# Performance work log

Hardware: AMD Instinct MI355X
Metric: run time of the kernel (lower is better)

The kernel has to match this reference:

```python
import jax, jax.numpy as jnp
import numpy as np

# Modulated deformable conv2d (torchvision semantics): per kernel tap, sample the
# input at a runtime-offset location via bilinear interpolation (zero padding
# outside the image), modulate with mask, then do the weighted accumulation.

STRIDE = (1, 1)
PADDING = (1, 1)
DILATION = (1, 1)


def deform_conv2d(x, offset, mask, weight, bias):
    B, C, H, W = x.shape
    O, Cg, kh, kw = weight.shape
    K = kh * kw
    og = offset.shape[1] // (2 * K)          # offset groups
    Ho, Wo = offset.shape[2], offset.shape[3]
    sh, sw = STRIDE
    ph, pw = PADDING
    dh, dw = DILATION

    off = offset.reshape(B, og, K, 2, Ho, Wo)
    ki = jnp.arange(K)
    base_ky = ((ki // kw) * dh).astype(x.dtype)            # [K]
    base_kx = ((ki % kw) * dw).astype(x.dtype)
    base_h = (jnp.arange(Ho) * sh - ph).astype(x.dtype)    # [Ho]
    base_w = (jnp.arange(Wo) * sw - pw).astype(x.dtype)    # [Wo]
    # sampling positions, [B, og, K, Ho, Wo]
    p_y = off[:, :, :, 0] + base_ky[None, None, :, None, None] + base_h[None, None, None, :, None]
    p_x = off[:, :, :, 1] + base_kx[None, None, :, None, None] + base_w[None, None, None, None, :]

    y0 = jnp.floor(p_y)
    x0 = jnp.floor(p_x)
    ly = p_y - y0
    lx = p_x - x0
    y0i = y0.astype(jnp.int32)
    x0i = x0.astype(jnp.int32)

    Cog = C // og
    x_flat = x.reshape(B, og, Cog, H * W)

    def gather(yi, xi):
        valid = ((yi >= 0) & (yi < H) & (xi >= 0) & (xi < W))
        idx = jnp.clip(yi, 0, H - 1) * W + jnp.clip(xi, 0, W - 1)
        idx_flat = idx.reshape(B, og, 1, K * Ho * Wo)
        v = jnp.take_along_axis(x_flat, idx_flat, axis=3).reshape(B, og, Cog, K, Ho, Wo)
        return v * valid[:, :, None].astype(x.dtype)

    w00 = ((1 - ly) * (1 - lx))[:, :, None]
    w01 = ((1 - ly) * lx)[:, :, None]
    w10 = (ly * (1 - lx))[:, :, None]
    w11 = (ly * lx)[:, :, None]
    val = (w00 * gather(y0i, x0i) + w01 * gather(y0i, x0i + 1)
           + w10 * gather(y0i + 1, x0i) + w11 * gather(y0i + 1, x0i + 1))

    if mask is not None:
        val = val * mask.reshape(B, og, K, Ho, Wo)[:, :, None]

    # grouped conv accumulation over sampled taps
    G = C // Cg                               # conv groups (=1 here)
    val = val.reshape(B, G, C // G, K, Ho, Wo)
    w = weight.reshape(G, O // G, Cg, K)
    out = jnp.einsum('bgckhw,gock->bgohw', val, w).reshape(B, O, Ho, Wo)
    if bias is not None:
        out = out + bias[None, :, None, None]
    return out


def setup_inputs() -> dict:
    key = jax.random.key(0)
    k1, k2, k3, k4, k5 = jax.random.split(key, 5)
    B, C, H, W = 4, 64, 128, 128
    O, kh, kw = 64, 3, 3
    return {
        'input': jax.random.normal(k1, (B, C, H, W), dtype=jnp.float32),
        'offset': jax.random.normal(k2, (B, 2 * kh * kw, H, W), dtype=jnp.float32),
        'mask': jax.random.uniform(k3, (B, kh * kw, H, W), dtype=jnp.float32),
        'weight': jax.random.normal(k4, (O, C, kh, kw), dtype=jnp.float32) * (1.0 / np.sqrt(C * kh * kw)),
        'bias': jax.random.normal(k5, (O,), dtype=jnp.float32) * 0.01,
    }


def reference(input, offset, mask, weight, bias):
    return deform_conv2d(input, offset, mask, weight, bias)
```

## Files before the change

### kernel.cpp

```cpp
#include <hip/hip_runtime.h>


#define BB 4
#define CC 64
#define HH 128
#define WW 128
#define OO 64
#define KHW 3
#define KK 9
#define HW (HH * WW)

typedef __bf16 bf16_t;
typedef bf16_t bf16x8 __attribute__((ext_vector_type(8)));
typedef float f32x4 __attribute__((ext_vector_type(4)));

__global__ __launch_bounds__(256) void nhwc_kernel(const float* __restrict__ x,
                                                   bf16_t* __restrict__ xt) {
    __shared__ float tile[64 * 65];
    const int t  = threadIdx.x;
    const int b  = blockIdx.x >> 8;
    const int p0 = (blockIdx.x & 255) << 6;
#pragma unroll
    for (int i = 0; i < 16; ++i) {
        int c = i * 4 + (t >> 6);
        int p = t & 63;
        tile[c * 65 + p] = x[(b * CC + c) * HW + p0 + p];
    }
    __syncthreads();
#pragma unroll
    for (int i = 0; i < 16; ++i) {
        int p = i * 4 + (t >> 6);
        int c = t & 63;
        xt[(size_t)((b * HW) + p0 + p) * CC + c] = (bf16_t)tile[c * 65 + p];
    }
}

__global__ void wfrag_kernel(const float* __restrict__ w,
                             bf16_t* __restrict__ wf) {
    int i = blockIdx.x * blockDim.x + threadIdx.x;
    if (i >= OO * CC * KK) return;
    int j    = i & 7;
    int lane = (i >> 3) & 63;
    int nt   = (i >> 9) & 3;
    int q    = (i >> 11) & 1;
    int k    = i >> 12;
    int o = nt * 16 + (lane & 15);
    int c = q * 32 + ((lane >> 4) << 3) + j;
    wf[i] = (bf16_t)w[(o * CC + c) * KK + k];
}

__global__ __launch_bounds__(256) void deform_conv_mfma(
    const bf16_t* __restrict__ xt, const float* __restrict__ offset,
    const float* __restrict__ mask, const bf16x8* __restrict__ wf,
    const float* __restrict__ bias, float* __restrict__ out) {
    const int t    = threadIdx.x;
    const int b    = blockIdx.x >> 8;
    const int p0   = (blockIdx.x & 255) << 6;
    const int lane = t & 63;
    const int wv   = t >> 6;
    const int m0   = wv << 4;
    const int col  = lane & 15;
    const int quad = lane >> 4;
    const int rem  = p0 + m0 + col;
    const int ho   = rem >> 7;
    const int wo   = rem & (WW - 1);
    const int cb   = quad << 3;

    const bf16_t* xb  = xt + (size_t)b * HW * CC;
    const float* offp = offset + (size_t)b * (2 * KK) * HW + rem;
    const float* mp   = mask + (size_t)b * KK * HW + rem;

    f32x4 acc[4];
#pragma unroll
    for (int nt = 0; nt < 4; ++nt) acc[nt] = (f32x4){0.f, 0.f, 0.f, 0.f};

    float offy = offp[0];
    float offx = offp[HW];
    float mm   = mp[0];

    for (int k = 0; k < KK; ++k) {
        float n_offy = 0.f, n_offx = 0.f, n_mm = 0.f;
        if (k < KK - 1) {
            n_offy = offp[(2 * k + 2) * HW];
            n_offx = offp[(2 * k + 3) * HW];
            n_mm   = mp[(k + 1) * HW];
        }

        float py = offy + (float)(k / KHW) + (float)(ho - 1);
        float px = offx + (float)(k % KHW) + (float)(wo - 1);
        float fy0 = floorf(py), fx0 = floorf(px);
        float ly = py - fy0, lx = px - fx0;
        int y0 = (int)fy0, x0 = (int)fx0;
        int y1 = y0 + 1, x1 = x0 + 1;
        bool vy0 = (y0 >= 0) && (y0 < HH);
        bool vy1 = (y1 >= 0) && (y1 < HH);
        bool vx0 = (x0 >= 0) && (x0 < WW);
        bool vx1 = (x1 >= 0) && (x1 < WW);
        int cy0 = min(max(y0, 0), HH - 1), cy1 = min(max(y1, 0), HH - 1);
        int cx0 = min(max(x0, 0), WW - 1), cx1 = min(max(x1, 0), WW - 1);
        float w0 = (vy0 && vx0) ? mm * (1.0f - ly) * (1.0f - lx) : 0.0f;
        float w1 = (vy0 && vx1) ? mm * (1.0f - ly) * lx : 0.0f;
        float w2 = (vy1 && vx0) ? mm * ly * (1.0f - lx) : 0.0f;
        float w3 = (vy1 && vx1) ? mm * ly * lx : 0.0f;

        const bf16_t* b00 = xb + (size_t)(cy0 * WW + cx0) * CC + cb;
        const bf16_t* b01 = xb + (size_t)(cy0 * WW + cx1) * CC + cb;
        const bf16_t* b10 = xb + (size_t)(cy1 * WW + cx0) * CC + cb;
        const bf16_t* b11 = xb + (size_t)(cy1 * WW + cx1) * CC + cb;
        bf16x8 a00 = *(const bf16x8*)b00, c00 = *(const bf16x8*)(b00 + 32);
        bf16x8 a01 = *(const bf16x8*)b01, c01 = *(const bf16x8*)(b01 + 32);
        bf16x8 a10 = *(const bf16x8*)b10, c10 = *(const bf16x8*)(b10 + 32);
        bf16x8 a11 = *(const bf16x8*)b11, c11 = *(const bf16x8*)(b11 + 32);

        bf16x8 af0, af1;
#pragma unroll
        for (int i = 0; i < 8; ++i) {
            float v = w0 * (float)a00[i] + w1 * (float)a01[i] +
                      w2 * (float)a10[i] + w3 * (float)a11[i];
            af0[i] = (bf16_t)v;
        }
#pragma unroll
        for (int i = 0; i < 8; ++i) {
            float v = w0 * (float)c00[i] + w1 * (float)c01[i] +
                      w2 * (float)c10[i] + w3 * (float)c11[i];
            af1[i] = (bf16_t)v;
        }

#pragma unroll
        for (int nt = 0; nt < 4; ++nt) {
            bf16x8 bfg = wf[(k * 8 + nt) * 64 + lane];
            acc[nt] = __builtin_amdgcn_mfma_f32_16x16x32_bf16(
                af0, bfg, acc[nt], 0, 0, 0);
        }
#pragma unroll
        for (int nt = 0; nt < 4; ++nt) {
            bf16x8 bfg = wf[(k * 8 + 4 + nt) * 64 + lane];
            acc[nt] = __builtin_amdgcn_mfma_f32_16x16x32_bf16(
                af1, bfg, acc[nt], 0, 0, 0);
        }

        offy = n_offy;
        offx = n_offx;
        mm   = n_mm;
    }

#pragma unroll
    for (int nt = 0; nt < 4; ++nt) {
        int o = nt * 16 + col;
        float bv = bias[o];
        f32x4 r = acc[nt];
        r.x += bv; r.y += bv; r.z += bv; r.w += bv;
        float* dst = out + (size_t)(b * OO + o) * HW + p0 + m0 + quad * 4;
        *(f32x4*)dst = r;
    }
}

extern "C" void kernel_launch(void* const* d_in, const int* in_sizes, int n_in,
                              void* d_out, int out_size, void* d_ws,
                              size_t ws_size, hipStream_t stream) {
    const float* x      = (const float*)d_in[0];
    const float* offset = (const float*)d_in[1];
    const float* mask   = (const float*)d_in[2];
    const float* weight = (const float*)d_in[3];
    const float* bias   = (const float*)d_in[4];
    float* out = (float*)d_out;

    bf16_t* xt  = (bf16_t*)d_ws;
    bf16_t* wfr = (bf16_t*)((char*)d_ws + (size_t)BB * HW * CC * 2);

    nhwc_kernel<<<BB * (HW / 64), 256, 0, stream>>>(x, xt);

    int nw = OO * CC * KK;
    wfrag_kernel<<<(nw + 255) / 256, 256, 0, stream>>>(weight, wfr);

    deform_conv_mfma<<<BB * (HW / 64), 256, 0, stream>>>(
        xt, offset, mask, (const bf16x8*)wfr, bias, out);
}
```

Measured before the change: 122.6 us.

## Split channel halves across wave pairs with LDS reduction; merge prep kernels

The main kernel now runs 512 threads per block, and each pair of waves splits the 64 input channels into two halves. Each wave gathers and interpolates only 32 channels and issues half the MFMAs, so more waves are available to hide gather latency. Partial accumulators are summed through shared memory before the bias add and store. The NHWC transpose and the weight-fragment kernels are also fused into one launch to save launch overhead. The cost is duplicated offset and mask loads and bilinear weight math per wave pair, plus a block-wide sync and LDS traffic.

Measured after the change: 126.4 us. 3.0% more time.

```diff
diff --git a/kernel.cpp b/kernel.cpp
--- a/kernel.cpp
+++ b/kernel.cpp
@@ -14,57 +14,60 @@
 typedef bf16_t bf16x8 __attribute__((ext_vector_type(8)));
 typedef float f32x4 __attribute__((ext_vector_type(4)));
 
-__global__ __launch_bounds__(256) void nhwc_kernel(const float* __restrict__ x,
-                                                   bf16_t* __restrict__ xt) {
+__global__ __launch_bounds__(256) void prep_kernel(const float* __restrict__ x,
+                                                   bf16_t* __restrict__ xt,
+                                                   const float* __restrict__ w,
+                                                   bf16_t* __restrict__ wf) {
     __shared__ float tile[64 * 65];
-    const int t  = threadIdx.x;
-    const int b  = blockIdx.x >> 8;
-    const int p0 = (blockIdx.x & 255) << 6;
+    const int t = threadIdx.x;
+    if (blockIdx.x < BB * 256) {
+        const int b  = blockIdx.x >> 8;
+        const int p0 = (blockIdx.x & 255) << 6;
 #pragma unroll
-    for (int i = 0; i < 16; ++i) {
-        int c = i * 4 + (t >> 6);
-        int p = t & 63;
-        tile[c * 65 + p] = x[(b * CC + c) * HW + p0 + p];
-    }
-    __syncthreads();
+        for (int i = 0; i < 16; ++i) {
+            int c = i * 4 + (t >> 6);
+            int p = t & 63;
+            tile[c * 65 + p] = x[(b * CC + c) * HW + p0 + p];
+        }
+        __syncthreads();
 #pragma unroll
-    for (int i = 0; i < 16; ++i) {
-        int p = i * 4 + (t >> 6);
-        int c = t & 63;
-        xt[(size_t)((b * HW) + p0 + p) * CC + c] = (bf16_t)tile[c * 65 + p];
+        for (int i = 0; i < 16; ++i) {
+            int p = i * 4 + (t >> 6);
+            int c = t & 63;
+            xt[(size_t)((b * HW) + p0 + p) * CC + c] = (bf16_t)tile[c * 65 + p];
+        }
+    } else {
+        int i = (blockIdx.x - BB * 256) * 256 + t;
+        if (i >= OO * CC * KK) return;
+        int j    = i & 7;
+        int lane = (i >> 3) & 63;
+        int nt   = (i >> 9) & 3;
+        int q    = (i >> 11) & 1;
+        int k    = i >> 12;
+        int o = nt * 16 + (lane & 15);
+        int c = q * 32 + ((lane >> 4) << 3) + j;
+        wf[i] = (bf16_t)w[(o * CC + c) * KK + k];
     }
 }
 
-__global__ void wfrag_kernel(const float* __restrict__ w,
-                             bf16_t* __restrict__ wf) {
-    int i = blockIdx.x * blockDim.x + threadIdx.x;
-    if (i >= OO * CC * KK) return;
-    int j    = i & 7;
-    int lane = (i >> 3) & 63;
-    int nt   = (i >> 9) & 3;
-    int q    = (i >> 11) & 1;
-    int k    = i >> 12;
-    int o = nt * 16 + (lane & 15);
-    int c = q * 32 + ((lane >> 4) << 3) + j;
-    wf[i] = (bf16_t)w[(o * CC + c) * KK + k];
-}
-
-__global__ __launch_bounds__(256) void deform_conv_mfma(
+__global__ __launch_bounds__(512, 8) void deform_conv_mfma(
     const bf16_t* __restrict__ xt, const float* __restrict__ offset,
     const float* __restrict__ mask, const bf16x8* __restrict__ wf,
     const float* __restrict__ bias, float* __restrict__ out) {
-    const int t    = threadIdx.x;
-    const int b    = blockIdx.x >> 8;
-    const int p0   = (blockIdx.x & 255) << 6;
-    const int lane = t & 63;
-    const int wv   = t >> 6;
-    const int m0   = wv << 4;
-    const int col  = lane & 15;
-    const int quad = lane >> 4;
-    const int rem  = p0 + m0 + col;
-    const int ho   = rem >> 7;
-    const int wo   = rem & (WW - 1);
-    const int cb   = quad << 3;
+    const int t     = threadIdx.x;
+    const int b     = blockIdx.x >> 8;
+    const int p0    = (blockIdx.x & 255) << 6;
+    const int lane  = t & 63;
+    const int wv    = t >> 6;
+    const int strip = wv >> 1;
+    const int q     = wv & 1;
+    const int m0    = strip << 4;
+    const int col   = lane & 15;
+    const int quad  = lane >> 4;
+    const int rem   = p0 + m0 + col;
+    const int ho    = rem >> 7;
+    const int wo    = rem & (WW - 1);
+    const int cb    = q * 32 + (quad << 3);
 
     const bf16_t* xb  = xt + (size_t)b * HW * CC;
     const float* offp = offset + (size_t)b * (2 * KK) * HW + rem;
@@ -103,40 +106,24 @@
         float w2 = (vy1 && vx0) ? mm * ly * (1.0f - lx) : 0.0f;
         float w3 = (vy1 && vx1) ? mm * ly * lx : 0.0f;
 
-        const bf16_t* b00 = xb + (size_t)(cy0 * WW + cx0) * CC + cb;
-        const bf16_t* b01 = xb + (size_t)(cy0 * WW + cx1) * CC + cb;
-        const bf16_t* b10 = xb + (size_t)(cy1 * WW + cx0) * CC + cb;
-        const bf16_t* b11 = xb + (size_t)(cy1 * WW + cx1) * CC + cb;
-        bf16x8 a00 = *(const bf16x8*)b00, c00 = *(const bf16x8*)(b00 + 32);
-        bf16x8 a01 = *(const bf16x8*)b01, c01 = *(const bf16x8*)(b01 + 32);
-        bf16x8 a10 = *(const bf16x8*)b10, c10 = *(const bf16x8*)(b10 + 32);
-        bf16x8 a11 = *(const bf16x8*)b11, c11 = *(const bf16x8*)(b11 + 32);
+        bf16x8 a00 = *(const bf16x8*)(xb + (size_t)(cy0 * WW + cx0) * CC + cb);
+        bf16x8 a01 = *(const bf16x8*)(xb + (size_t)(cy0 * WW + cx1) * CC + cb);
+        bf16x8 a10 = *(const bf16x8*)(xb + (size_t)(cy1 * WW + cx0) * CC + cb);
+        bf16x8 a11 = *(const bf16x8*)(xb + (size_t)(cy1 * WW + cx1) * CC + cb);
 
-        bf16x8 af0, af1;
+        bf16x8 af;
 #pragma unroll
         for (int i = 0; i < 8; ++i) {
             float v = w0 * (float)a00[i] + w1 * (float)a01[i] +
                       w2 * (float)a10[i] + w3 * (float)a11[i];
-            af0[i] = (bf16_t)v;
-        }
-#pragma unroll
-        for (int i = 0; i < 8; ++i) {
-            float v = w0 * (float)c00[i] + w1 * (float)c01[i] +
-                      w2 * (float)c10[i] + w3 * (float)c11[i];
-            af1[i] = (bf16_t)v;
+            af[i] = (bf16_t)v;
         }
 
 #pragma unroll
         for (int nt = 0; nt < 4; ++nt) {
-            bf16x8 bfg = wf[(k * 8 + nt) * 64 + lane];
+            bf16x8 bfg = wf[((k * 2 + q) * 4 + nt) * 64 + lane];
             acc[nt] = __builtin_amdgcn_mfma_f32_16x16x32_bf16(
-                af0, bfg, acc[nt], 0, 0, 0);
-        }
-#pragma unroll
-        for (int nt = 0; nt < 4; ++nt) {
-            bf16x8 bfg = wf[(k * 8 + 4 + nt) * 64 + lane];
-            acc[nt] = __builtin_amdgcn_mfma_f32_16x16x32_bf16(
-                af1, bfg, acc[nt], 0, 0, 0);
+                af, bfg, acc[nt], 0, 0, 0);
         }
 
         offy = n_offy;
@@ -144,14 +131,22 @@
         mm   = n_mm;
     }
 
+    __shared__ f32x4 red[4][64][4];
+    if (q) {
 #pragma unroll
-    for (int nt = 0; nt < 4; ++nt) {
-        int o = nt * 16 + col;
-        float bv = bias[o];
-        f32x4 r = acc[nt];
-        r.x += bv; r.y += bv; r.z += bv; r.w += bv;
-        float* dst = out + (size_t)(b * OO + o) * HW + p0 + m0 + quad * 4;
-        *(f32x4*)dst = r;
+        for (int nt = 0; nt < 4; ++nt) red[strip][lane][nt] = acc[nt];
+    }
+    __syncthreads();
+    if (!q) {
+#pragma unroll
+        for (int nt = 0; nt < 4; ++nt) {
+            int o = nt * 16 + col;
+            float bv = bias[o];
+            f32x4 r = acc[nt] + red[strip][lane][nt];
+            r.x += bv; r.y += bv; r.z += bv; r.w += bv;
+            float* dst = out + (size_t)(b * OO + o) * HW + p0 + m0 + quad * 4;
+            *(f32x4*)dst = r;
+        }
     }
 }
 
@@ -168,11 +163,9 @@
     bf16_t* xt  = (bf16_t*)d_ws;
     bf16_t* wfr = (bf16_t*)((char*)d_ws + (size_t)BB * HW * CC * 2);
 
-    nhwc_kernel<<<BB * (HW / 64), 256, 0, stream>>>(x, xt);
+    int nwf_blocks = (OO * CC * KK + 255) / 256;
+    prep_kernel<<<BB * 256 + nwf_blocks, 256, 0, stream>>>(x, xt, weight, wfr);
 
-    int nw = OO * CC * KK;
-    wfrag_kernel<<<(nw + 255) / 256, 256, 0, stream>>>(weight, wfr);
-
-    deform_conv_mfma<<<BB * (HW / 64), 256, 0, stream>>>(
+    deform_conv_mfma<<<BB * (HW / 64), 512, 0, stream>>>(
         xt, offset, mask, (const bf16x8*)wfr, bias, out);
 }
```

## Software-pipeline gathers across taps, merge prep kernels, swizzle block order

Applied to the files above, without the earlier changes.

Restructures the tap loop into a fully unrolled two-stage software pipeline: the bilinear gather loads for tap k+1 and the offset/mask loads for tap k+2 are issued before tap k is blended and fed to the MFMAs, so gather latency overlaps compute. It also merges the NHWC transpose and weight-fragment kernels into a single launch, adds a min-blocks-per-CU hint to launch_bounds, and reorders block indices with a stride-8 interleave. The double-buffered registers raise register pressure, which the occupancy hint may force into spills.

Result: no change. 121.5 us (-0.9%).

```diff
diff --git a/kernel.cpp b/kernel.cpp
--- a/kernel.cpp
+++ b/kernel.cpp
@@ -14,48 +14,50 @@
 typedef bf16_t bf16x8 __attribute__((ext_vector_type(8)));
 typedef float f32x4 __attribute__((ext_vector_type(4)));
 
-__global__ __launch_bounds__(256) void nhwc_kernel(const float* __restrict__ x,
-                                                   bf16_t* __restrict__ xt) {
+__global__ __launch_bounds__(256) void prep_kernel(const float* __restrict__ x,
+                                                   bf16_t* __restrict__ xt,
+                                                   const float* __restrict__ w,
+                                                   bf16_t* __restrict__ wf) {
     __shared__ float tile[64 * 65];
-    const int t  = threadIdx.x;
-    const int b  = blockIdx.x >> 8;
-    const int p0 = (blockIdx.x & 255) << 6;
-#pragma unroll
-    for (int i = 0; i < 16; ++i) {
-        int c = i * 4 + (t >> 6);
-        int p = t & 63;
-        tile[c * 65 + p] = x[(b * CC + c) * HW + p0 + p];
-    }
-    __syncthreads();
-#pragma unroll
-    for (int i = 0; i < 16; ++i) {
-        int p = i * 4 + (t >> 6);
-        int c = t & 63;
-        xt[(size_t)((b * HW) + p0 + p) * CC + c] = (bf16_t)tile[c * 65 + p];
+    const int t = threadIdx.x;
+    if (blockIdx.x < BB * 256) {
+        const int b  = blockIdx.x >> 8;
+        const int p0 = (blockIdx.x & 255) << 6;
+#pragma unroll
+        for (int i = 0; i < 16; ++i) {
+            int c = i * 4 + (t >> 6);
+            int p = t & 63;
+            tile[c * 65 + p] = x[(b * CC + c) * HW + p0 + p];
+        }
+        __syncthreads();
+#pragma unroll
+        for (int i = 0; i < 16; ++i) {
+            int p = i * 4 + (t >> 6);
+            int c = t & 63;
+            xt[(size_t)((b * HW) + p0 + p) * CC + c] = (bf16_t)tile[c * 65 + p];
+        }
+    } else {
+        int i = (blockIdx.x - BB * 256) * 256 + t;
+        if (i >= OO * CC * KK) return;
+        int j    = i & 7;
+        int lane = (i >> 3) & 63;
+        int nt   = (i >> 9) & 3;
+        int q    = (i >> 11) & 1;
+        int k    = i >> 12;
+        int o = nt * 16 + (lane & 15);
+        int c = q * 32 + ((lane >> 4) << 3) + j;
+        wf[i] = (bf16_t)w[(o * CC + c) * KK + k];
     }
 }
 
-__global__ void wfrag_kernel(const float* __restrict__ w,
-                             bf16_t* __restrict__ wf) {
-    int i = blockIdx.x * blockDim.x + threadIdx.x;
-    if (i >= OO * CC * KK) return;
-    int j    = i & 7;
-    int lane = (i >> 3) & 63;
-    int nt   = (i >> 9) & 3;
-    int q    = (i >> 11) & 1;
-    int k    = i >> 12;
-    int o = nt * 16 + (lane & 15);
-    int c = q * 32 + ((lane >> 4) << 3) + j;
-    wf[i] = (bf16_t)w[(o * CC + c) * KK + k];
-}
-
-__global__ __launch_bounds__(256) void deform_conv_mfma(
+__global__ __launch_bounds__(256, 4) void deform_conv_mfma(
     const bf16_t* __restrict__ xt, const float* __restrict__ offset,
     const float* __restrict__ mask, const bf16x8* __restrict__ wf,
     const float* __restrict__ bias, float* __restrict__ out) {
     const int t    = threadIdx.x;
-    const int b    = blockIdx.x >> 8;
-    const int p0   = (blockIdx.x & 255) << 6;
+    const int wg   = (blockIdx.x & 7) * ((BB * 256) >> 3) + (blockIdx.x >> 3);
+    const int b    = wg >> 8;
+    const int p0   = (wg & 255) << 6;
     const int lane = t & 63;
     const int wv   = t >> 6;
     const int m0   = wv << 4;
@@ -65,6 +67,8 @@
     const int ho   = rem >> 7;
     const int wo   = rem & (WW - 1);
     const int cb   = quad << 3;
+    const float fho = (float)(ho - 1);
+    const float fwo = (float)(wo - 1);
 
     const bf16_t* xb  = xt + (size_t)b * HW * CC;
     const float* offp = offset + (size_t)b * (2 * KK) * HW + rem;
@@ -74,75 +78,105 @@
 #pragma unroll
     for (int nt = 0; nt < 4; ++nt) acc[nt] = (f32x4){0.f, 0.f, 0.f, 0.f};
 
-    float offy = offp[0];
-    float offx = offp[HW];
-    float mm   = mp[0];
-
-    for (int k = 0; k < KK; ++k) {
-        float n_offy = 0.f, n_offx = 0.f, n_mm = 0.f;
-        if (k < KK - 1) {
-            n_offy = offp[(2 * k + 2) * HW];
-            n_offx = offp[(2 * k + 3) * HW];
-            n_mm   = mp[(k + 1) * HW];
-        }
-
-        float py = offy + (float)(k / KHW) + (float)(ho - 1);
-        float px = offx + (float)(k % KHW) + (float)(wo - 1);
-        float fy0 = floorf(py), fx0 = floorf(px);
-        float ly = py - fy0, lx = px - fx0;
-        int y0 = (int)fy0, x0 = (int)fx0;
-        int y1 = y0 + 1, x1 = x0 + 1;
-        bool vy0 = (y0 >= 0) && (y0 < HH);
-        bool vy1 = (y1 >= 0) && (y1 < HH);
-        bool vx0 = (x0 >= 0) && (x0 < WW);
-        bool vx1 = (x1 >= 0) && (x1 < WW);
-        int cy0 = min(max(y0, 0), HH - 1), cy1 = min(max(y1, 0), HH - 1);
-        int cx0 = min(max(x0, 0), WW - 1), cx1 = min(max(x1, 0), WW - 1);
-        float w0 = (vy0 && vx0) ? mm * (1.0f - ly) * (1.0f - lx) : 0.0f;
-        float w1 = (vy0 && vx1) ? mm * (1.0f - ly) * lx : 0.0f;
-        float w2 = (vy1 && vx0) ? mm * ly * (1.0f - lx) : 0.0f;
-        float w3 = (vy1 && vx1) ? mm * ly * lx : 0.0f;
-
-        const bf16_t* b00 = xb + (size_t)(cy0 * WW + cx0) * CC + cb;
-        const bf16_t* b01 = xb + (size_t)(cy0 * WW + cx1) * CC + cb;
-        const bf16_t* b10 = xb + (size_t)(cy1 * WW + cx0) * CC + cb;
-        const bf16_t* b11 = xb + (size_t)(cy1 * WW + cx1) * CC + cb;
-        bf16x8 a00 = *(const bf16x8*)b00, c00 = *(const bf16x8*)(b00 + 32);
-        bf16x8 a01 = *(const bf16x8*)b01, c01 = *(const bf16x8*)(b01 + 32);
-        bf16x8 a10 = *(const bf16x8*)b10, c10 = *(const bf16x8*)(b10 + 32);
-        bf16x8 a11 = *(const bf16x8*)b11, c11 = *(const bf16x8*)(b11 + 32);
-
-        bf16x8 af0, af1;
-#pragma unroll
-        for (int i = 0; i < 8; ++i) {
-            float v = w0 * (float)a00[i] + w1 * (float)a01[i] +
-                      w2 * (float)a10[i] + w3 * (float)a11[i];
-            af0[i] = (bf16_t)v;
-        }
-#pragma unroll
-        for (int i = 0; i < 8; ++i) {
-            float v = w0 * (float)c00[i] + w1 * (float)c01[i] +
-                      w2 * (float)c10[i] + w3 * (float)c11[i];
-            af1[i] = (bf16_t)v;
-        }
-
-#pragma unroll
-        for (int nt = 0; nt < 4; ++nt) {
-            bf16x8 bfg = wf[(k * 8 + nt) * 64 + lane];
-            acc[nt] = __builtin_amdgcn_mfma_f32_16x16x32_bf16(
-                af0, bfg, acc[nt], 0, 0, 0);
-        }
-#pragma unroll
-        for (int nt = 0; nt < 4; ++nt) {
-            bf16x8 bfg = wf[(k * 8 + 4 + nt) * 64 + lane];
-            acc[nt] = __builtin_amdgcn_mfma_f32_16x16x32_bf16(
-                af1, bfg, acc[nt], 0, 0, 0);
-        }
-
-        offy = n_offy;
-        offx = n_offx;
-        mm   = n_mm;
-    }
+    float syA, sxA, smA, syB, sxB, smB;
+    float wA0, wA1, wA2, wA3, wB0, wB1, wB2, wB3;
+    bf16x8 gA00, gA01, gA10, gA11, hA00, hA01, hA10, hA11;
+    bf16x8 gB00, gB01, gB10, gB11, hB00, hB01, hB10, hB11;
+    bf16x8 af0, af1;
+
+#define LOADS(k_, P_)                                                         \
+    if ((k_) < KK) {                                                          \
+        sy##P_ = offp[(2 * (k_)) * HW];                                       \
+        sx##P_ = offp[(2 * (k_) + 1) * HW];                                   \
+        sm##P_ = mp[(k_) * HW];                                               \
+    }
+
+#define ISSUE(k_, P_)                                                         \
+    {                                                                         \
+        float py = sy##P_ + (float)((k_) / KHW) + fho;                        \
+        float px = sx##P_ + (float)((k_) % KHW) + fwo;                        \
+        float fy0 = floorf(py), fx0 = floorf(px);                             \
+        float ly = py - fy0, lx = px - fx0;                                   \
+        int y0 = (int)fy0, x0 = (int)fx0;                                     \
+        int y1 = y0 + 1, x1 = x0 + 1;                                         \
+        bool vy0 = (y0 >= 0) && (y0 < HH), vy1 = (y1 >= 0) && (y1 < HH);      \
+        bool vx0 = (x0 >= 0) && (x0 < WW), vx1 = (x1 >= 0) && (x1 < WW);      \
+        int cy0 = min(max(y0, 0), HH - 1), cy1 = min(max(y1, 0), HH - 1);     \
+        int cx0 = min(max(x0, 0), WW - 1), cx1 = min(max(x1, 0), WW - 1);     \
+        float mmv = sm##P_;                                                   \
+        w##P_##0 = (vy0 && vx0) ? mmv * (1.0f - ly) * (1.0f - lx) : 0.0f;     \
+        w##P_##1 = (vy0 && vx1) ? mmv * (1.0f - ly) * lx : 0.0f;              \
+        w##P_##2 = (vy1 && vx0) ? mmv * ly * (1.0f - lx) : 0.0f;              \
+        w##P_##3 = (vy1 && vx1) ? mmv * ly * lx : 0.0f;                       \
+        const bf16_t* b00 = xb + (size_t)(cy0 * WW + cx0) * CC + cb;          \
+        const bf16_t* b01 = xb + (size_t)(cy0 * WW + cx1) * CC + cb;          \
+        const bf16_t* b10 = xb + (size_t)(cy1 * WW + cx0) * CC + cb;          \
+        const bf16_t* b11 = xb + (size_t)(cy1 * WW + cx1) * CC + cb;          \
+        g##P_##00 = *(const bf16x8*)b00; h##P_##00 = *(const bf16x8*)(b00 + 32); \
+        g##P_##01 = *(const bf16x8*)b01; h##P_##01 = *(const bf16x8*)(b01 + 32); \
+        g##P_##10 = *(const bf16x8*)b10; h##P_##10 = *(const bf16x8*)(b10 + 32); \
+        g##P_##11 = *(const bf16x8*)b11; h##P_##11 = *(const bf16x8*)(b11 + 32); \
+    }
+
+#define BLEND(P_)                                                             \
+    {                                                                         \
+        _Pragma("unroll") for (int i = 0; i < 8; ++i) {                       \
+            float v = w##P_##0 * (float)g##P_##00[i] +                        \
+                      w##P_##1 * (float)g##P_##01[i] +                        \
+                      w##P_##2 * (float)g##P_##10[i] +                        \
+                      w##P_##3 * (float)g##P_##11[i];                         \
+            af0[i] = (bf16_t)v;                                               \
+        }                                                                     \
+        _Pragma("unroll") for (int i = 0; i < 8; ++i) {                       \
+            float v = w##P_##0 * (float)h##P_##00[i] +                        \
+                      w##P_##1 * (float)h##P_##01[i] +                        \
+                      w##P_##2 * (float)h##P_##10[i] +                        \
+                      w##P_##3 * (float)h##P_##11[i];                         \
+            af1[i] = (bf16_t)v;                                               \
+        }                                                                     \
+    }
+
+#define MFMAS(k_)                                                             \
+    {                                                                         \
+        _Pragma("unroll") for (int nt = 0; nt < 4; ++nt) {                    \
+            bf16x8 bfg = wf[((k_) * 8 + nt) * 64 + lane];                     \
+            acc[nt] = __builtin_amdgcn_mfma_f32_16x16x32_bf16(                \
+                af0, bfg, acc[nt], 0, 0, 0);                                  \
+        }                                                                     \
+        _Pragma("unroll") for (int nt = 0; nt < 4; ++nt) {                    \
+            bf16x8 bfg = wf[((k_) * 8 + 4 + nt) * 64 + lane];                 \
+            acc[nt] = __builtin_amdgcn_mfma_f32_16x16x32_bf16(                \
+                af1, bfg, acc[nt], 0, 0, 0);                                  \
+        }                                                                     \
+    }
+
+#define BODY(k_, P_, Q_)                                                      \
+    {                                                                         \
+        if ((k_) + 1 < KK) ISSUE((k_) + 1, Q_);                               \
+        LOADS((k_) + 2, P_);                                                  \
+        BLEND(P_);                                                            \
+        MFMAS(k_);                                                            \
+    }
+
+    LOADS(0, A)
+    LOADS(1, B)
+    ISSUE(0, A);
+
+    BODY(0, A, B)
+    BODY(1, B, A)
+    BODY(2, A, B)
+    BODY(3, B, A)
+    BODY(4, A, B)
+    BODY(5, B, A)
+    BODY(6, A, B)
+    BODY(7, B, A)
+    BODY(8, A, B)
+
+#undef BODY
+#undef MFMAS
+#undef BLEND
+#undef ISSUE
+#undef LOADS
 
 #pragma unroll
     for (int nt = 0; nt < 4; ++nt) {
@@ -168,10 +202,8 @@
     bf16_t* xt  = (bf16_t*)d_ws;
     bf16_t* wfr = (bf16_t*)((char*)d_ws + (size_t)BB * HW * CC * 2);
 
-    nhwc_kernel<<<BB * (HW / 64), 256, 0, stream>>>(x, xt);
-
-    int nw = OO * CC * KK;
-    wfrag_kernel<<<(nw + 255) / 256, 256, 0, stream>>>(weight, wfr);
+    int nwf_blocks = (OO * CC * KK + 255) / 256;
+    prep_kernel<<<BB * 256 + nwf_blocks, 256, 0, stream>>>(x, xt, weight, wfr);
 
     deform_conv_mfma<<<BB * (HW / 64), 256, 0, stream>>>(
         xt, offset, mask, (const bf16x8*)wfr, bias, out);
```

## Stage 16x16 halo input window in LDS with 8x8 spatial tiles and fallback gathers

Applied to the files above, without the earlier changes.

Each workgroup now covers an 8x8 output tile instead of a 64-pixel row segment. It loads a swizzled 16x16 NHWC bf16 halo window into shared memory, and bilinear taps read from LDS, falling back to global loads only for samples outside the window. The two prep kernels are merged into one launch, workgroup ids are remapped across XCDs, and the tap loop is fully unrolled with an occupancy hint. In exchange there is 32KB of LDS per block, which limits occupancy, plus divergent fallback loads when offsets are large.

After: 100.1 us. 18.4% less time.

```diff
diff --git a/kernel.cpp b/kernel.cpp
--- a/kernel.cpp
+++ b/kernel.cpp
@@ -14,62 +14,83 @@
 typedef bf16_t bf16x8 __attribute__((ext_vector_type(8)));
 typedef float f32x4 __attribute__((ext_vector_type(4)));
 
-__global__ __launch_bounds__(256) void nhwc_kernel(const float* __restrict__ x,
-                                                   bf16_t* __restrict__ xt) {
+__global__ __launch_bounds__(256) void prep_kernel(const float* __restrict__ x,
+                                                   bf16_t* __restrict__ xt,
+                                                   const float* __restrict__ w,
+                                                   bf16_t* __restrict__ wf) {
     __shared__ float tile[64 * 65];
-    const int t  = threadIdx.x;
-    const int b  = blockIdx.x >> 8;
-    const int p0 = (blockIdx.x & 255) << 6;
-#pragma unroll
-    for (int i = 0; i < 16; ++i) {
-        int c = i * 4 + (t >> 6);
-        int p = t & 63;
-        tile[c * 65 + p] = x[(b * CC + c) * HW + p0 + p];
-    }
-    __syncthreads();
-#pragma unroll
-    for (int i = 0; i < 16; ++i) {
-        int p = i * 4 + (t >> 6);
-        int c = t & 63;
-        xt[(size_t)((b * HW) + p0 + p) * CC + c] = (bf16_t)tile[c * 65 + p];
+    const int t = threadIdx.x;
+    if (blockIdx.x < BB * 256) {
+        const int b  = blockIdx.x >> 8;
+        const int p0 = (blockIdx.x & 255) << 6;
+#pragma unroll
+        for (int i = 0; i < 16; ++i) {
+            int c = i * 4 + (t >> 6);
+            int p = t & 63;
+            tile[c * 65 + p] = x[(b * CC + c) * HW + p0 + p];
+        }
+        __syncthreads();
+#pragma unroll
+        for (int i = 0; i < 16; ++i) {
+            int p = i * 4 + (t >> 6);
+            int c = t & 63;
+            xt[(size_t)((b * HW) + p0 + p) * CC + c] = (bf16_t)tile[c * 65 + p];
+        }
+    } else {
+        int i = (blockIdx.x - BB * 256) * 256 + t;
+        if (i >= OO * CC * KK) return;
+        int j    = i & 7;
+        int lane = (i >> 3) & 63;
+        int nt   = (i >> 9) & 3;
+        int q    = (i >> 11) & 1;
+        int k    = i >> 12;
+        int o = nt * 16 + (lane & 15);
+        int c = q * 32 + ((lane >> 4) << 3) + j;
+        wf[i] = (bf16_t)w[(o * CC + c) * KK + k];
     }
 }
 
-__global__ void wfrag_kernel(const float* __restrict__ w,
-                             bf16_t* __restrict__ wf) {
-    int i = blockIdx.x * blockDim.x + threadIdx.x;
-    if (i >= OO * CC * KK) return;
-    int j    = i & 7;
-    int lane = (i >> 3) & 63;
-    int nt   = (i >> 9) & 3;
-    int q    = (i >> 11) & 1;
-    int k    = i >> 12;
-    int o = nt * 16 + (lane & 15);
-    int c = q * 32 + ((lane >> 4) << 3) + j;
-    wf[i] = (bf16_t)w[(o * CC + c) * KK + k];
-}
-
-__global__ __launch_bounds__(256) void deform_conv_mfma(
+__global__ __launch_bounds__(256, 4) void deform_conv_mfma(
     const bf16_t* __restrict__ xt, const float* __restrict__ offset,
     const float* __restrict__ mask, const bf16x8* __restrict__ wf,
     const float* __restrict__ bias, float* __restrict__ out) {
     const int t    = threadIdx.x;
-    const int b    = blockIdx.x >> 8;
-    const int p0   = (blockIdx.x & 255) << 6;
+    const int wg   = (blockIdx.x & 7) * ((BB * 256) >> 3) + (blockIdx.x >> 3);
+    const int b    = wg >> 8;
+    const int ti   = wg & 255;
+    const int r0   = ((ti >> 4) << 3);
+    const int c0   = ((ti & 15) << 3);
     const int lane = t & 63;
     const int wv   = t >> 6;
-    const int m0   = wv << 4;
     const int col  = lane & 15;
     const int quad = lane >> 4;
-    const int rem  = p0 + m0 + col;
-    const int ho   = rem >> 7;
-    const int wo   = rem & (WW - 1);
+    const int prow = r0 + 2 * wv + (col >> 3);
+    const int pcol = c0 + (col & 7);
+    const int rem  = prow * WW + pcol;
+    const int wy0  = r0 - 4;
+    const int wx0  = c0 - 4;
     const int cb   = quad << 3;
+
+    __shared__ bf16_t V[256 * 64];
 
     const bf16_t* xb  = xt + (size_t)b * HW * CC;
     const float* offp = offset + (size_t)b * (2 * KK) * HW + rem;
     const float* mp   = mask + (size_t)b * KK * HW + rem;
 
+    {
+        const int i  = t >> 4;
+        const int j  = t & 15;
+        const int cy = min(max(wy0 + i, 0), HH - 1);
+        const int cx = min(max(wx0 + j, 0), WW - 1);
+        const bf16_t* src = xb + (size_t)(cy * WW + cx) * CC;
+        bf16_t* dst = &V[(i * 16 + j) * 64];
+        const int sw = (j & 7) * 8;
+#pragma unroll
+        for (int s = 0; s < 8; ++s)
+            *(bf16x8*)(dst + ((s * 8) ^ sw)) = *(const bf16x8*)(src + s * 8);
+    }
+    __syncthreads();
+
     f32x4 acc[4];
 #pragma unroll
     for (int nt = 0; nt < 4; ++nt) acc[nt] = (f32x4){0.f, 0.f, 0.f, 0.f};
@@ -78,6 +99,7 @@
     float offx = offp[HW];
     float mm   = mp[0];
 
+#pragma unroll
     for (int k = 0; k < KK; ++k) {
         float n_offy = 0.f, n_offx = 0.f, n_mm = 0.f;
         if (k < KK - 1) {
@@ -86,16 +108,14 @@
             n_mm   = mp[(k + 1) * HW];
         }
 
-        float py = offy + (float)(k / KHW) + (float)(ho - 1);
-        float px = offx + (float)(k % KHW) + (float)(wo - 1);
+        float py = offy + (float)(k / KHW) + (float)(prow - 1);
+        float px = offx + (float)(k % KHW) + (float)(pcol - 1);
         float fy0 = floorf(py), fx0 = floorf(px);
         float ly = py - fy0, lx = px - fx0;
         int y0 = (int)fy0, x0 = (int)fx0;
         int y1 = y0 + 1, x1 = x0 + 1;
-        bool vy0 = (y0 >= 0) && (y0 < HH);
-        bool vy1 = (y1 >= 0) && (y1 < HH);
-        bool vx0 = (x0 >= 0) && (x0 < WW);
-        bool vx1 = (x1 >= 0) && (x1 < WW);
+        bool vy0 = (y0 >= 0) && (y0 < HH), vy1 = (y1 >= 0) && (y1 < HH);
+        bool vx0 = (x0 >= 0) && (x0 < WW), vx1 = (x1 >= 0) && (x1 < WW);
         int cy0 = min(max(y0, 0), HH - 1), cy1 = min(max(y1, 0), HH - 1);
         int cx0 = min(max(x0, 0), WW - 1), cx1 = min(max(x1, 0), WW - 1);
         float w0 = (vy0 && vx0) ? mm * (1.0f - ly) * (1.0f - lx) : 0.0f;
@@ -103,26 +123,53 @@
         float w2 = (vy1 && vx0) ? mm * ly * (1.0f - lx) : 0.0f;
         float w3 = (vy1 && vx1) ? mm * ly * lx : 0.0f;
 
-        const bf16_t* b00 = xb + (size_t)(cy0 * WW + cx0) * CC + cb;
-        const bf16_t* b01 = xb + (size_t)(cy0 * WW + cx1) * CC + cb;
-        const bf16_t* b10 = xb + (size_t)(cy1 * WW + cx0) * CC + cb;
-        const bf16_t* b11 = xb + (size_t)(cy1 * WW + cx1) * CC + cb;
-        bf16x8 a00 = *(const bf16x8*)b00, c00 = *(const bf16x8*)(b00 + 32);
-        bf16x8 a01 = *(const bf16x8*)b01, c01 = *(const bf16x8*)(b01 + 32);
-        bf16x8 a10 = *(const bf16x8*)b10, c10 = *(const bf16x8*)(b10 + 32);
-        bf16x8 a11 = *(const bf16x8*)b11, c11 = *(const bf16x8*)(b11 + 32);
+        int uy0 = y0 - wy0, ux0 = x0 - wx0;
+        int uy1 = uy0 + 1,  ux1 = ux0 + 1;
+        bool iy0 = (unsigned)uy0 < 16u, iy1 = (unsigned)uy1 < 16u;
+        bool ix0 = (unsigned)ux0 < 16u, ix1 = (unsigned)ux1 < 16u;
+        int qy0 = min(max(uy0, 0), 15), qy1 = min(max(uy1, 0), 15);
+        int qx0 = min(max(ux0, 0), 15), qx1 = min(max(ux1, 0), 15);
+        int pa = (qy0 * 16 + qx0) * 64, pb = (qy0 * 16 + qx1) * 64;
+        int pc = (qy1 * 16 + qx0) * 64, pd = (qy1 * 16 + qx1) * 64;
+        int sa = (qx0 & 7), sb = (qx1 & 7);
+
+        bf16x8 g00 = *(const bf16x8*)&V[pa + ((quad ^ sa) << 3)];
+        bf16x8 h00 = *(const bf16x8*)&V[pa + (((4 + quad) ^ sa) << 3)];
+        bf16x8 g01 = *(const bf16x8*)&V[pb + ((quad ^ sb) << 3)];
+        bf16x8 h01 = *(const bf16x8*)&V[pb + (((4 + quad) ^ sb) << 3)];
+        bf16x8 g10 = *(const bf16x8*)&V[pc + ((quad ^ sa) << 3)];
+        bf16x8 h10 = *(const bf16x8*)&V[pc + (((4 + quad) ^ sa) << 3)];
+        bf16x8 g11 = *(const bf16x8*)&V[pd + ((quad ^ sb) << 3)];
+        bf16x8 h11 = *(const bf16x8*)&V[pd + (((4 + quad) ^ sb) << 3)];
+
+        if (w0 != 0.0f && !(iy0 && ix0)) {
+            const bf16_t* p = xb + (size_t)(cy0 * WW + cx0) * CC + cb;
+            g00 = *(const bf16x8*)p; h00 = *(const bf16x8*)(p + 32);
+        }
+        if (w1 != 0.0f && !(iy0 && ix1)) {
+            const bf16_t* p = xb + (size_t)(cy0 * WW + cx1) * CC + cb;
+            g01 = *(const bf16x8*)p; h01 = *(const bf16x8*)(p + 32);
+        }
+        if (w2 != 0.0f && !(iy1 && ix0)) {
+            const bf16_t* p = xb + (size_t)(cy1 * WW + cx0) * CC + cb;
+            g10 = *(const bf16x8*)p; h10 = *(const bf16x8*)(p + 32);
+        }
+        if (w3 != 0.0f && !(iy1 && ix1)) {
+            const bf16_t* p = xb + (size_t)(cy1 * WW + cx1) * CC + cb;
+            g11 = *(const bf16x8*)p; h11 = *(const bf16x8*)(p + 32);
+        }
 
         bf16x8 af0, af1;
 #pragma unroll
         for (int i = 0; i < 8; ++i) {
-            float v = w0 * (float)a00[i] + w1 * (float)a01[i] +
-                      w2 * (float)a10[i] + w3 * (float)a11[i];
+            float v = w0 * (float)g00[i] + w1 * (float)g01[i] +
+                      w2 * (float)g10[i] + w3 * (float)g11[i];
             af0[i] = (bf16_t)v;
         }
 #pragma unroll
         for (int i = 0; i < 8; ++i) {
-            float v = w0 * (float)c00[i] + w1 * (float)c01[i] +
-                      w2 * (float)c10[i] + w3 * (float)c11[i];
+            float v = w0 * (float)h00[i] + w1 * (float)h01[i] +
+                      w2 * (float)h10[i] + w3 * (float)h11[i];
             af1[i] = (bf16_t)v;
         }
 
@@ -150,7 +197,8 @@
         float bv = bias[o];
         f32x4 r = acc[nt];
         r.x += bv; r.y += bv; r.z += bv; r.w += bv;
-        float* dst = out + (size_t)(b * OO + o) * HW + p0 + m0 + quad * 4;
+        float* dst = out + (size_t)(b * OO + o) * HW +
+                     (r0 + 2 * wv + (quad >> 1)) * WW + c0 + (quad & 1) * 4;
         *(f32x4*)dst = r;
     }
 }
@@ -168,10 +216,8 @@
     bf16_t* xt  = (bf16_t*)d_ws;
     bf16_t* wfr = (bf16_t*)((char*)d_ws + (size_t)BB * HW * CC * 2);
 
-    nhwc_kernel<<<BB * (HW / 64), 256, 0, stream>>>(x, xt);
-
-    int nw = OO * CC * KK;
-    wfrag_kernel<<<(nw + 255) / 256, 256, 0, stream>>>(weight, wfr);
+    int nwf_blocks = (OO * CC * KK + 255) / 256;
+    prep_kernel<<<BB * 256 + nwf_blocks, 256, 0, stream>>>(x, xt, weight, wfr);
 
     deform_conv_mfma<<<BB * (HW / 64), 256, 0, stream>>>(
         xt, offset, mask, (const bf16x8*)wfr, bias, out);
```
